# Kernel tuning notes

Hardware: AMD Instinct MI355X
Metric: run time of the kernel (lower is better)

The kernel has to match this reference:

```python
import jax, jax.numpy as jnp
import numpy as np

B, L, LQ = 64, 4096, 128
D = 32        # input_dim (value channels)
ET = 128      # embed_time
NH = 1        # num_heads
H = 128       # nhidden
NC = 6        # n_classes


def _time_emb(tt, lin_w, lin_b, per_w, per_b):
    # tt [..., T] -> [..., T, ET]; cat(Linear(1,1)(t), sin(Linear(1,ET-1)(t)))
    tt = tt[..., None]
    out1 = tt * lin_w[0, 0] + lin_b
    out2 = jnp.sin(tt @ per_w + per_b)
    return jnp.concatenate([out1, out2], axis=-1)


def _gru_dir(xs, wih, whh, bih, bhh, reverse):
    # xs [B, T, I] -> [B, T, H]; torch GRU gate math
    xs_t = jnp.swapaxes(xs, 0, 1)              # [T, B, I]
    if reverse:
        xs_t = xs_t[::-1]
    gi_all = xs_t @ wih.T + bih                # [T, B, 3H] precomputed input gates
    h0 = jnp.zeros((xs.shape[0], H), xs.dtype)

    def step(h, gi):
        gh = h @ whh.T + bhh
        ir, iz, inn = jnp.split(gi, 3, axis=-1)
        hr, hz, hn = jnp.split(gh, 3, axis=-1)
        r = jax.nn.sigmoid(ir + hr)
        z = jax.nn.sigmoid(iz + hz)
        n = jnp.tanh(inn + r * hn)
        h_new = (1.0 - z) * n + z * h
        return h_new, h_new

    _, ys = jax.lax.scan(step, h0, gi_all)     # [T, B, H]
    if reverse:
        ys = ys[::-1]
    return jnp.swapaxes(ys, 0, 1)


def _bigru(xs, wih, whh, bih, bhh):
    fwd = _gru_dir(xs, wih[0], whh[0], bih[0], bhh[0], False)
    bwd = _gru_dir(xs, wih[1], whh[1], bih[1], bhh[1], True)
    return jnp.concatenate([fwd, bwd], axis=-1)


def setup_inputs() -> dict:
    ks = jax.random.split(jax.random.key(0), 32)
    w = lambda i, s: jax.random.normal(ks[i], s, jnp.float32) * 0.05
    G3 = 3 * H
    return {
        "x": jax.random.normal(ks[0], (B, L, D), jnp.float32),
        "time_steps": jax.random.uniform(ks[1], (B, L), dtype=jnp.float32),
        "query_times": jnp.linspace(0.0, 1.0, LQ, dtype=jnp.float32),
        "lin_w": w(2, (1, 1)), "lin_b": w(3, (1,)),
        "per_w": w(4, (1, ET - 1)), "per_b": w(5, (ET - 1,)),
        "wq": w(6, (ET, ET)), "bq": w(7, (ET,)),
        "wk": w(8, (ET, ET)), "bk": w(9, (ET,)),
        "wo": w(10, (NH * D, H)), "bo": w(11, (H,)),
        "gru0_wih": w(12, (2, G3, H)), "gru0_whh": w(13, (2, G3, H)),
        "gru0_bih": w(14, (2, G3)), "gru0_bhh": w(15, (2, G3)),
        "gru1_wih": w(16, (2, G3, 2 * H)), "gru1_whh": w(17, (2, G3, H)),
        "gru1_bih": w(18, (2, G3)), "gru1_bhh": w(19, (2, G3)),
        "c1_w": w(20, (2 * H, 128)), "c1_b": w(21, (128,)),
        "c2_w": w(22, (128, 64)), "c2_b": w(23, (64,)),
        "c3_w": w(24, (64, NC)), "c3_b": w(25, (NC,)),
    }


def reference(x, time_steps, query_times, lin_w, lin_b, per_w, per_b,
              wq, bq, wk, bk, wo, bo,
              gru0_wih, gru0_whh, gru0_bih, gru0_bhh,
              gru1_wih, gru1_whh, gru1_bih, gru1_bhh,
              c1_w, c1_b, c2_w, c2_b, c3_w, c3_b):
    ek = ET // NH
    # learned time embeddings
    q = _time_emb(query_times[None, :], lin_w, lin_b, per_w, per_b)  # [1, LQ, ET]
    k = _time_emb(time_steps, lin_w, lin_b, per_w, per_b)            # [B, L, ET]
    # per-head projections
    qp = (q @ wq + bq).reshape(1, LQ, NH, ek).transpose(0, 2, 1, 3)[0]  # [NH, LQ, ek]
    kp = (k @ wk + bk).reshape(B, L, NH, ek).transpose(0, 2, 1, 3)      # [B, NH, L, ek]
    # mTAN attention: scores are channel-independent (mask=None), so the
    # per-channel repeat+softmax reduces to a single softmax over keys.
    scores = jnp.einsum('hqe,bhke->bhqk', qp, kp) / jnp.sqrt(jnp.float32(ek))
    p = jax.nn.softmax(scores, axis=-1)                                 # [B, NH, LQ, L]
    att = jnp.einsum('bhqk,bkd->bqhd', p, x).reshape(B, LQ, NH * D)
    att_out = att @ wo + bo                                             # [B, LQ, H]
    # 2-layer bidirectional GRU
    g0 = _bigru(att_out, gru0_wih, gru0_whh, gru0_bih, gru0_bhh)        # [B, LQ, 2H]
    g1 = _bigru(g0, gru1_wih, gru1_whh, gru1_bih, gru1_bhh)             # [B, LQ, 2H]
    class_in = jnp.concatenate([g1[:, -1, :H], g1[:, 0, H:]], axis=1)   # [B, 2H]
    out = ((class_in @ c1_w + c1_b) @ c2_w + c2_b) @ c3_w + c3_b        # [B, NC]
    return out
```

## Files before the change

### kernel.cpp

```cpp
#include <hip/hip_runtime.h>
#include <math.h>

#define Bn   64
#define Ln   4096
#define LQn  128
#define Dn   32
#define ETn  128
#define Hn   128
#define G3n  384
#define NDEG 12

typedef __attribute__((ext_vector_type(2))) float f32x2;
typedef __attribute__((ext_vector_type(2))) _Float16 f16x2;

#define DPPF(x, ctrl) __int_as_float(__builtin_amdgcn_update_dpp(0, __float_as_int(x), (ctrl), 0xF, 0xF, true))
#define QP_XOR1 0xB1
#define QP_XOR2 0x4E
#define QP_B0   0x00
#define QP_B1   0x55
#define QP_B2   0xAA
#define QP_B3   0xFF

__device__ __forceinline__ float sin_poly(float x) {
    const float x2 = x * x;
    float r = -1.9841270114e-04f;
    r = fmaf(r, x2,  8.3333337680e-03f);
    r = fmaf(r, x2, -1.6666667163e-01f);
    return fmaf(r * x2, x, x);
}
__device__ __forceinline__ float cos_poly(float x) {
    const float x2 = x * x;
    float r =  2.4801587642e-05f;
    r = fmaf(r, x2, -1.3888888899e-03f);
    r = fmaf(r, x2,  4.1666667908e-02f);
    r = fmaf(r, x2, -5.0000000000e-01f);
    return fmaf(r, x2, 1.0f);
}

#define WS_C    0
#define WS_WT   4096
#define WS_B2   (WS_WT + 768*32)
#define WS_CLS  (WS_B2 + 1024)
#define WS_G0   (WS_CLS + Bn*2*Hn)
#define WS_GI   (WS_G0 + Bn*LQn*2*Hn)
#define WS_ACCP WS_G0
#define WS_SP   (WS_G0 + 1048576)

__global__ __launch_bounds__(128) void k_coef(
    const float* __restrict__ qtimes, const float* __restrict__ lin_w,
    const float* __restrict__ lin_b, const float* __restrict__ per_w,
    const float* __restrict__ per_b, const float* __restrict__ wq,
    const float* __restrict__ bq, const float* __restrict__ wk,
    const float* __restrict__ bk, float* __restrict__ C)
{
    __shared__ float qe[ETn], qp_l[ETn], qt_l[ETn], bas[NDEG * 128], red[96], qbk_red[32];
    const int q = blockIdx.x, tid = threadIdx.x;
    if (tid < ETn - 1) {
        const float w = per_w[tid], bb = per_b[tid];
        const float sb = sin_poly(bb), cb = cos_poly(bb);
        float wp = 1.f;
#pragma unroll
        for (int d = 0; d < NDEG; ++d) {
            const float sd = ((d & 3) == 0) ? sb : ((d & 3) == 1) ? cb : ((d & 3) == 2) ? -sb : -cb;
            bas[d * 128 + tid] = wp * sd;
            wp *= w / (float)(d + 1);
        }
    }
    const float t = qtimes[q];
    qe[tid] = (tid == 0) ? fmaf(t, lin_w[0], lin_b[0])
                         : sin_poly(fmaf(t, per_w[tid - 1], per_b[tid - 1]));
    __syncthreads();
    {
        float a = bq[tid];
#pragma unroll 16
        for (int i = 0; i < ETn; ++i) a = fmaf(qe[i], wq[i * ETn + tid], a);
        qp_l[tid] = a;
    }
    __syncthreads();
    {
        const float4* wk4 = (const float4*)(wk + (size_t)tid * ETn);
        const float4* qp4 = (const float4*)qp_l;
        float a = 0.f;
#pragma unroll
        for (int k = 0; k < 32; ++k) {
            const float4 w4 = wk4[k], p4 = qp4[k];
            a += w4.x * p4.x + w4.y * p4.y + w4.z * p4.z + w4.w * p4.w;
        }
        qt_l[tid] = a;
    }
    __syncthreads();
    if (tid < 96) {
        const int d = tid >> 3, g = tid & 7;
        float p = 0.f;
        for (int j = g; j < ETn - 1; j += 8) p = fmaf(qt_l[j + 1], bas[d * 128 + j], p);
        red[tid] = p;
    } else {
        const int g2 = tid - 96;
        float p = 0.f;
#pragma unroll
        for (int k = 0; k < 4; ++k) p = fmaf(qp_l[g2 + 32 * k], bk[g2 + 32 * k], p);
        qbk_red[g2] = p;
    }
    __syncthreads();
    if (tid < NDEG) {
        const int d = tid;
        float s = red[d * 8 + 0] + red[d * 8 + 1] + red[d * 8 + 2] + red[d * 8 + 3]
                + red[d * 8 + 4] + red[d * 8 + 5] + red[d * 8 + 6] + red[d * 8 + 7];
        if (d == 0) {
            float qbk = 0.f;
#pragma unroll
            for (int k = 0; k < 32; ++k) qbk += qbk_red[k];
            s += qt_l[0] * lin_b[0] + qbk;
        }
        if (d == 1) s += qt_l[0] * lin_w[0];
        C[q * NDEG + d] = s * 0.08838834764831845f;
    }
}

__global__ __launch_bounds__(256) void k_fuse(
    const float* __restrict__ wih, const float* __restrict__ wo,
    const float* __restrict__ bo, const float* __restrict__ bih,
    float* __restrict__ Wt, float* __restrict__ bias2)
{
    const int t = blockIdx.x * 256 + threadIdx.x;
    if (t < 768 * 32) {
        const int o = t >> 5, d = t & 31;
        const float4* wr4 = (const float4*)(wih + (size_t)o * 128);
        const float4* wc4 = (const float4*)(wo + (size_t)d * 128);
        float a = 0.f;
#pragma unroll
        for (int k = 0; k < 32; ++k) {
            const float4 r4 = wr4[k], c4 = wc4[k];
            a += r4.x * c4.x + r4.y * c4.y + r4.z * c4.z + r4.w * c4.w;
        }
        Wt[t] = a;
    } else if (t < 768 * 33) {
        const int o = t - 768 * 32;
        const float4* wr4 = (const float4*)(wih + (size_t)o * 128);
        const float4* bo4 = (const float4*)bo;
        float a = bih[o];
#pragma unroll
        for (int k = 0; k < 32; ++k) {
            const float4 r4 = wr4[k], b4 = bo4[k];
            a += r4.x * b4.x + r4.y * b4.y + r4.z * b4.z + r4.w * b4.w;
        }
        bias2[o] = a;
    }
}

__global__ __launch_bounds__(512, 4) void k_attn(
    const float* __restrict__ x, const float* __restrict__ tsteps,
    const float* __restrict__ Cc, float* __restrict__ accP, float* __restrict__ sP)
{
    __shared__ __align__(16) char smem[4 * 128 * 36 * 4];
    float4* xls  = (float4*)smem;
    float*  slabf = (float*)smem;
#define SLAB(s, qq, c) slabf[(((s) * 128) + (qq)) * 36 + (c)]
    const int tid = threadIdx.x;
    const int b = blockIdx.x >> 2, lsplit = blockIdx.x & 3;
    const int i = tid & 3, qt = (tid >> 2) & 31, ls2 = tid >> 7;
    const int qown = 4 * qt + i;
    const int u = tid & 127;

    float c[NDEG];
#pragma unroll
    for (int d = 0; d < NDEG; ++d) c[d] = Cc[qown * NDEG + d];

    const int l0 = lsplit * 1024 + ls2 * 256;
    const float4* tg4 = (const float4*)(tsteps + (size_t)b * Ln + l0);
    const float4* xg  = (const float4*)(x + ((size_t)b * Ln + l0) * Dn);

    f32x2 acc2[4][4];
#pragma unroll
    for (int m = 0; m < 4; ++m)
#pragma unroll
        for (int e = 0; e < 4; ++e) { acc2[m][e].x = 0.f; acc2[m][e].y = 0.f; }
    float s_own = 0.f;

    float4 xr[4];
#pragma unroll
    for (int w = 0; w < 4; ++w) xr[w] = xg[u + 128 * w];

    for (int ch = 0; ch < 4; ++ch) {
        __syncthreads();
#pragma unroll
        for (int w = 0; w < 4; ++w) xls[ls2 * 512 + u + 128 * w] = xr[w];
        __syncthreads();
        if (ch < 3) {
            const int off = (ch + 1) * 512;
#pragma unroll
            for (int w = 0; w < 4; ++w) xr[w] = xg[off + u + 128 * w];
        }
        const float4* xrow = &xls[ls2 * 512];
        for (int k = 0; k < 16; ++k) {
            const float4 t4 = tg4[ch * 16 + k];
#pragma unroll
            for (int jj = 0; jj < 4; ++jj) {
                const float t = (jj == 0) ? t4.x : (jj == 1) ? t4.y : (jj == 2) ? t4.z : t4.w;
                float sc = c[NDEG - 1];
#pragma unroll
                for (int d = NDEG - 2; d >= 0; --d) sc = fmaf(sc, t, c[d]);
                const float pe = __expf(sc);
                s_own += pe;
                const float p0 = DPPF(pe, QP_B0);
                const float p1 = DPPF(pe, QP_B1);
                const float p2 = DPPF(pe, QP_B2);
                const float p3 = DPPF(pe, QP_B3);
                const int lrow = (k * 4 + jj) * 8;
                const float4 xa = xrow[lrow + 2 * i];
                const float4 xb = xrow[lrow + 2 * i + 1];
                f32x2 xa0; xa0.x = xa.x; xa0.y = xa.y;
                f32x2 xa1; xa1.x = xa.z; xa1.y = xa.w;
                f32x2 xb0; xb0.x = xb.x; xb0.y = xb.y;
                f32x2 xb1; xb1.x = xb.z; xb1.y = xb.w;
#define PKA(m, pv) { f32x2 pp; pp.x = (pv); pp.y = (pv); \
    acc2[m][0] = __builtin_elementwise_fma(pp, xa0, acc2[m][0]); \
    acc2[m][1] = __builtin_elementwise_fma(pp, xa1, acc2[m][1]); \
    acc2[m][2] = __builtin_elementwise_fma(pp, xb0, acc2[m][2]); \
    acc2[m][3] = __builtin_elementwise_fma(pp, xb1, acc2[m][3]); }
                PKA(0, p0) PKA(1, p1) PKA(2, p2) PKA(3, p3)
#undef PKA
            }
        }
    }
    __syncthreads();
#pragma unroll
    for (int m = 0; m < 4; ++m) {
        float4 f4a, f4b;
        f4a.x = acc2[m][0].x; f4a.y = acc2[m][0].y; f4a.z = acc2[m][1].x; f4a.w = acc2[m][1].y;
        f4b.x = acc2[m][2].x; f4b.y = acc2[m][2].y; f4b.z = acc2[m][3].x; f4b.w = acc2[m][3].y;
        *(float4*)&SLAB(ls2, 4 * qt + m, 8 * i)     = f4a;
        *(float4*)&SLAB(ls2, 4 * qt + m, 8 * i + 4) = f4b;
    }
    SLAB(ls2, qown, 32) = s_own;
    __syncthreads();
    const int q = tid & 127, part = tid >> 7;
#pragma unroll
    for (int j = 0; j < 2; ++j) {
        const int off = (part * 2 + j) * 4;
        float4 r  = *(float4*)&SLAB(0, q, off);
        float4 r1 = *(float4*)&SLAB(1, q, off);
        float4 r2 = *(float4*)&SLAB(2, q, off);
        float4 r3 = *(float4*)&SLAB(3, q, off);
        r.x += r1.x + r2.x + r3.x; r.y += r1.y + r2.y + r3.y;
        r.z += r1.z + r2.z + r3.z; r.w += r1.w + r2.w + r3.w;
        *(float4*)&accP[((((size_t)lsplit * Bn + b) * LQn + q) * 32) + off] = r;
    }
    if (part == 0) {
        sP[((size_t)lsplit * Bn + b) * LQn + q] =
            SLAB(0, q, 32) + SLAB(1, q, 32) + SLAB(2, q, 32) + SLAB(3, q, 32);
    }
#undef SLAB
}

__global__ __launch_bounds__(256) void k_gemm_att(
    const float* __restrict__ accP, const float* __restrict__ sP,
    const float* __restrict__ Bm, const float* __restrict__ bias,
    float* __restrict__ Cm)
{
    __shared__ float4 A_l[64 * 8];
    __shared__ float4 B_l[64 * 8];
    const int tid = threadIdx.x;
    const int m0 = blockIdx.x * 64, n0 = blockIdx.y * 64;
    const int r0 = (tid >> 4) << 2, c0 = (tid & 15) << 2;
    f32x2 acc2[4][4];
#pragma unroll
    for (int a = 0; a < 4; ++a)
#pragma unroll
        for (int bb = 0; bb < 4; ++bb) { acc2[a][bb].x = 0.f; acc2[a][bb].y = 0.f; }
    const float4* Ag = (const float4*)accP;
    const float4* Bg = (const float4*)Bm;

#pragma unroll
    for (int w = 0; w < 2; ++w) {
        const int idx = tid + w * 256;
        const int row = idx >> 3, c4 = idx & 7;
        const int sc = (c4 + row + (row >> 2)) & 7;
        const int m = m0 + row;
        float4 a0 = Ag[(size_t)m * 8 + c4];
        float4 a1 = Ag[((size_t)8192  + m) * 8 + c4];
        float4 a2 = Ag[((size_t)16384 + m) * 8 + c4];
        float4 a3 = Ag[((size_t)24576 + m) * 8 + c4];
        const float inv = 1.f / (sP[m] + sP[8192 + m] + sP[16384 + m] + sP[24576 + m]);
        float4 av;
        av.x = (a0.x + a1.x + a2.x + a3.x) * inv;
        av.y = (a0.y + a1.y + a2.y + a3.y) * inv;
        av.z = (a0.z + a1.z + a2.z + a3.z) * inv;
        av.w = (a0.w + a1.w + a2.w + a3.w) * inv;
        A_l[row * 8 + sc] = av;
        B_l[row * 8 + sc] = Bg[(size_t)(n0 + row) * 8 + c4];
    }
    __syncthreads();
#pragma unroll
    for (int k4 = 0; k4 < 8; ++k4) {
        float4 av[4], bv[4];
#pragma unroll
        for (int j = 0; j < 4; ++j) {
            const int ra = r0 + j;
            av[j] = A_l[ra * 8 + ((k4 + ra + (ra >> 2)) & 7)];
        }
#pragma unroll
        for (int j = 0; j < 4; ++j) {
            const int rb = c0 + j;
            bv[j] = B_l[rb * 8 + ((k4 + rb + (rb >> 2)) & 7)];
        }
#pragma unroll
        for (int ri = 0; ri < 4; ++ri) {
            f32x2 alo; alo.x = av[ri].x; alo.y = av[ri].y;
            f32x2 ahi; ahi.x = av[ri].z; ahi.y = av[ri].w;
#pragma unroll
            for (int ci = 0; ci < 4; ++ci) {
                f32x2 blo; blo.x = bv[ci].x; blo.y = bv[ci].y;
                f32x2 bhi; bhi.x = bv[ci].z; bhi.y = bv[ci].w;
                acc2[ri][ci] = __builtin_elementwise_fma(alo, blo, acc2[ri][ci]);
                acc2[ri][ci] = __builtin_elementwise_fma(ahi, bhi, acc2[ri][ci]);
            }
        }
    }
#pragma unroll
    for (int ri = 0; ri < 4; ++ri) {
        float4 o4;
        o4.x = acc2[ri][0].x + acc2[ri][0].y + bias[n0 + c0 + 0];
        o4.y = acc2[ri][1].x + acc2[ri][1].y + bias[n0 + c0 + 1];
        o4.z = acc2[ri][2].x + acc2[ri][2].y + bias[n0 + c0 + 2];
        o4.w = acc2[ri][3].x + acc2[ri][3].y + bias[n0 + c0 + 3];
        *(float4*)&Cm[(size_t)(m0 + r0 + ri) * 768 + n0 + c0] = o4;
    }
}

__global__ __launch_bounds__(256) void k_gemm_nt(
    const float* __restrict__ A, const float* __restrict__ Bm,
    const float* __restrict__ bias, float* __restrict__ Cm,
    int N, int K)
{
    __shared__ float4 A_l[64 * 8];
    __shared__ float4 B_l[64 * 8];
    const int tid = threadIdx.x;
    const int m0 = blockIdx.x * 64, n0 = blockIdx.y * 64;
    const int r0 = (tid >> 4) << 2, c0 = (tid & 15) << 2;
    const int K4 = K >> 2;
    f32x2 acc2[4][4];
#pragma unroll
    for (int a = 0; a < 4; ++a)
#pragma unroll
        for (int bb = 0; bb < 4; ++bb) { acc2[a][bb].x = 0.f; acc2[a][bb].y = 0.f; }
    const float4* Ag = (const float4*)A;
    const float4* Bg = (const float4*)Bm;

    for (int k0 = 0; k0 < K4; k0 += 8) {
        __syncthreads();
#pragma unroll
        for (int w = 0; w < 2; ++w) {
            const int idx = tid + w * 256;
            const int row = idx >> 3, c4 = idx & 7;
            const int sc = (c4 + row + (row >> 2)) & 7;
            A_l[row * 8 + sc] = Ag[(size_t)(m0 + row) * K4 + k0 + c4];
            B_l[row * 8 + sc] = Bg[(size_t)(n0 + row) * K4 + k0 + c4];
        }
        __syncthreads();
#pragma unroll
        for (int k4 = 0; k4 < 8; ++k4) {
            float4 av[4], bv[4];
#pragma unroll
            for (int j = 0; j < 4; ++j) {
                const int ra = r0 + j;
                av[j] = A_l[ra * 8 + ((k4 + ra + (ra >> 2)) & 7)];
            }
#pragma unroll
            for (int j = 0; j < 4; ++j) {
                const int rb = c0 + j;
                bv[j] = B_l[rb * 8 + ((k4 + rb + (rb >> 2)) & 7)];
            }
#pragma unroll
            for (int ri = 0; ri < 4; ++ri) {
                f32x2 alo; alo.x = av[ri].x; alo.y = av[ri].y;
                f32x2 ahi; ahi.x = av[ri].z; ahi.y = av[ri].w;
#pragma unroll
                for (int ci = 0; ci < 4; ++ci) {
                    f32x2 blo; blo.x = bv[ci].x; blo.y = bv[ci].y;
                    f32x2 bhi; bhi.x = bv[ci].z; bhi.y = bv[ci].w;
                    acc2[ri][ci] = __builtin_elementwise_fma(alo, blo, acc2[ri][ci]);
                    acc2[ri][ci] = __builtin_elementwise_fma(ahi, bhi, acc2[ri][ci]);
                }
            }
        }
    }
#pragma unroll
    for (int ri = 0; ri < 4; ++ri) {
        float4 o4;
        o4.x = acc2[ri][0].x + acc2[ri][0].y + bias[n0 + c0 + 0];
        o4.y = acc2[ri][1].x + acc2[ri][1].y + bias[n0 + c0 + 1];
        o4.z = acc2[ri][2].x + acc2[ri][2].y + bias[n0 + c0 + 2];
        o4.w = acc2[ri][3].x + acc2[ri][3].y + bias[n0 + c0 + 3];
        *(float4*)&Cm[(size_t)(m0 + r0 + ri) * N + n0 + c0] = o4;
    }
}

__global__ __launch_bounds__(256, 1) void k_gru(
    const float* __restrict__ gi, const float* __restrict__ whh,
    const float* __restrict__ bhh, float* __restrict__ seq_out,
    float* __restrict__ final_out)
{
    __shared__ _Float16 h16[2][Hn];
    __shared__ float    h32[2][Hn];
    const int tid = threadIdx.x;
    const int b = blockIdx.x >> 1, dir = blockIdx.x & 1;
    const int j = tid >> 1, q = tid & 1;

    f16x2 wr[32], wz[32], wn[32];
    {
        const float* wb = whh + ((size_t)dir * G3n + j) * Hn + 64 * q;
        const f32x2* p0 = (const f32x2*)(wb);
        const f32x2* p1 = (const f32x2*)(wb + (size_t)128 * Hn);
        const f32x2* p2 = (const f32x2*)(wb + (size_t)256 * Hn);
#pragma unroll
        for (int k = 0; k < 32; ++k) {
            f32x2 a = p0[k], z2 = p1[k], c2 = p2[k];
            wr[k].x = (_Float16)a.x;  wr[k].y = (_Float16)a.y;
            wz[k].x = (_Float16)z2.x; wz[k].y = (_Float16)z2.y;
            wn[k].x = (_Float16)c2.x; wn[k].y = (_Float16)c2.y;
        }
    }
#pragma unroll
    for (int k = 0; k < 32; ++k) {
        asm volatile("" : "+v"(wr[k]));
        asm volatile("" : "+v"(wz[k]));
        asm volatile("" : "+v"(wn[k]));
    }
    const float bhr = bhh[dir * G3n + j];
    const float bhz = bhh[dir * G3n + 128 + j];
    const float bhn = bhh[dir * G3n + 256 + j];

    if (tid < Hn) {
        h32[0][tid] = 0.f; h32[1][tid] = 0.f;
        h16[0][tid] = (_Float16)0.f; h16[1][tid] = (_Float16)0.f;
    }
    __syncthreads();

    const long sstride = dir ? -768 : 768;
    const float* gptr = gi + (size_t)b * LQn * 768 + dir * G3n + j
                        + (size_t)(dir ? LQn - 1 : 0) * 768;

    int cur = 0;
    float hlast = 0.f;

    auto gstep = [&](const float gir, const float giz, const float gin, const int step) {
        const float hold = h32[cur][j];
        const float4* hb4 = (const float4*)(&h16[cur][64 * q]);
        float srA = 0.f, szA = 0.f, snA = 0.f;
        float srB = 0.f, szB = 0.f, snB = 0.f;
#pragma unroll
        for (int k2 = 0; k2 < 4; ++k2) {
            float4 hv = hb4[k2];
            f16x2 h0 = *(f16x2*)&hv.x;
            f16x2 h1 = *(f16x2*)&hv.y;
            f16x2 h2 = *(f16x2*)&hv.z;
            f16x2 h3 = *(f16x2*)&hv.w;
            asm("v_dot2_f32_f16 %0, %1, %2, %0" : "+v"(srA) : "v"(wr[4 * k2 + 0]), "v"(h0));
            asm("v_dot2_f32_f16 %0, %1, %2, %0" : "+v"(szA) : "v"(wz[4 * k2 + 0]), "v"(h0));
            asm("v_dot2_f32_f16 %0, %1, %2, %0" : "+v"(snA) : "v"(wn[4 * k2 + 0]), "v"(h0));
            asm("v_dot2_f32_f16 %0, %1, %2, %0" : "+v"(srA) : "v"(wr[4 * k2 + 1]), "v"(h1));
            asm("v_dot2_f32_f16 %0, %1, %2, %0" : "+v"(szA) : "v"(wz[4 * k2 + 1]), "v"(h1));
            asm("v_dot2_f32_f16 %0, %1, %2, %0" : "+v"(snA) : "v"(wn[4 * k2 + 1]), "v"(h1));
            asm("v_dot2_f32_f16 %0, %1, %2, %0" : "+v"(srA) : "v"(wr[4 * k2 + 2]), "v"(h2));
            asm("v_dot2_f32_f16 %0, %1, %2, %0" : "+v"(szA) : "v"(wz[4 * k2 + 2]), "v"(h2));
            asm("v_dot2_f32_f16 %0, %1, %2, %0" : "+v"(snA) : "v"(wn[4 * k2 + 2]), "v"(h2));
            asm("v_dot2_f32_f16 %0, %1, %2, %0" : "+v"(srA) : "v"(wr[4 * k2 + 3]), "v"(h3));
            asm("v_dot2_f32_f16 %0, %1, %2, %0" : "+v"(szA) : "v"(wz[4 * k2 + 3]), "v"(h3));
            asm("v_dot2_f32_f16 %0, %1, %2, %0" : "+v"(snA) : "v"(wn[4 * k2 + 3]), "v"(h3));
        }
#pragma unroll
        for (int k2 = 4; k2 < 8; ++k2) {
            float4 hv = hb4[k2];
            f16x2 h0 = *(f16x2*)&hv.x;
            f16x2 h1 = *(f16x2*)&hv.y;
            f16x2 h2 = *(f16x2*)&hv.z;
            f16x2 h3 = *(f16x2*)&hv.w;
            asm("v_dot2_f32_f16 %0, %1, %2, %0" : "+v"(srB) : "v"(wr[4 * k2 + 0]), "v"(h0));
            asm("v_dot2_f32_f16 %0, %1, %2, %0" : "+v"(szB) : "v"(wz[4 * k2 + 0]), "v"(h0));
            asm("v_dot2_f32_f16 %0, %1, %2, %0" : "+v"(snB) : "v"(wn[4 * k2 + 0]), "v"(h0));
            asm("v_dot2_f32_f16 %0, %1, %2, %0" : "+v"(srB) : "v"(wr[4 * k2 + 1]), "v"(h1));
            asm("v_dot2_f32_f16 %0, %1, %2, %0" : "+v"(szB) : "v"(wz[4 * k2 + 1]), "v"(h1));
            asm("v_dot2_f32_f16 %0, %1, %2, %0" : "+v"(snB) : "v"(wn[4 * k2 + 1]), "v"(h1));
            asm("v_dot2_f32_f16 %0, %1, %2, %0" : "+v"(srB) : "v"(wr[4 * k2 + 2]), "v"(h2));
            asm("v_dot2_f32_f16 %0, %1, %2, %0" : "+v"(szB) : "v"(wz[4 * k2 + 2]), "v"(h2));
            asm("v_dot2_f32_f16 %0, %1, %2, %0" : "+v"(snB) : "v"(wn[4 * k2 + 2]), "v"(h2));
            asm("v_dot2_f32_f16 %0, %1, %2, %0" : "+v"(srB) : "v"(wr[4 * k2 + 3]), "v"(h3));
            asm("v_dot2_f32_f16 %0, %1, %2, %0" : "+v"(szB) : "v"(wz[4 * k2 + 3]), "v"(h3));
            asm("v_dot2_f32_f16 %0, %1, %2, %0" : "+v"(snB) : "v"(wn[4 * k2 + 3]), "v"(h3));
        }
        float sr = srA + srB, sz = szA + szB, sn = snA + snB;
        sr += DPPF(sr, QP_XOR1);
        sz += DPPF(sz, QP_XOR1);
        sn += DPPF(sn, QP_XOR1);
        const float r = 1.f / (1.f + __expf(-(gir + sr + bhr)));
        const float z = 1.f / (1.f + __expf(-(giz + sz + bhz)));
        const float nx = gin + r * (sn + bhn);
        const float n = 1.f - 2.f / (1.f + __expf(2.f * nx));
        const float hn = n + z * (hold - n);
        if (q == 0) {
            h32[cur ^ 1][j] = hn;
            h16[cur ^ 1][j] = (_Float16)hn;
            if (seq_out) {
                const int l = dir ? (LQn - 1 - step) : step;
                seq_out[((size_t)(b * LQn + l)) * (2 * Hn) + dir * Hn + j] = hn;
            }
        }
        hlast = hn;
        cur ^= 1;
        asm volatile("s_waitcnt lgkmcnt(0)\n\ts_barrier" ::: "memory");
    };

    float gA[3], gB[3];
#define GLD(dst, s) { const long o = (long)(s) * sstride; \
    dst[0] = gptr[o]; dst[1] = gptr[o + 128]; dst[2] = gptr[o + 256]; }
    GLD(gA, 0) GLD(gB, 1)
    for (int s0 = 0; s0 < LQn; s0 += 2) {
        gstep(gA[0], gA[1], gA[2], s0);
        { const int sn2 = (s0 + 2 < LQn) ? s0 + 2 : LQn - 1; GLD(gA, sn2) }
        gstep(gB[0], gB[1], gB[2], s0 + 1);
        { const int sn2 = (s0 + 3 < LQn) ? s0 + 3 : LQn - 1; GLD(gB, sn2) }
    }
#undef GLD
    if (final_out && q == 0) final_out[b * 2 * Hn + dir * Hn + j] = hlast;
}

__global__ __launch_bounds__(256) void k_cls(
    const float* __restrict__ cls_in,
    const float* __restrict__ c1w, const float* __restrict__ c1b,
    const float* __restrict__ c2w, const float* __restrict__ c2b,
    const float* __restrict__ c3w, const float* __restrict__ c3b,
    float* __restrict__ out)
{
    __shared__ float ci[256], y1[128], y2[64];
    const int b = blockIdx.x, tid = threadIdx.x;
    ci[tid] = cls_in[b * 256 + tid];
    __syncthreads();
    if (tid < 128) { float a = c1b[tid]; for (int i = 0; i < 256; ++i) a += ci[i] * c1w[i * 128 + tid]; y1[tid] = a; }
    __syncthreads();
    if (tid < 64)  { float a = c2b[tid]; for (int i = 0; i < 128; ++i) a += y1[i] * c2w[i * 64 + tid];  y2[tid] = a; }
    __syncthreads();
    if (tid < 6)   { float a = c3b[tid]; for (int i = 0; i < 64; ++i)  a += y2[i] * c3w[i * 6 + tid];   out[b * 6 + tid] = a; }
}

extern "C" void kernel_launch(void* const* d_in, const int* in_sizes, int n_in,
                              void* d_out, int out_size, void* d_ws, size_t ws_size,
                              hipStream_t stream)
{
    const float* x        = (const float*)d_in[0];
    const float* tsteps   = (const float*)d_in[1];
    const float* qtimes   = (const float*)d_in[2];
    const float* lin_w    = (const float*)d_in[3];
    const float* lin_b    = (const float*)d_in[4];
    const float* per_w    = (const float*)d_in[5];
    const float* per_b    = (const float*)d_in[6];
    const float* wq       = (const float*)d_in[7];
    const float* bq       = (const float*)d_in[8];
    const float* wk       = (const float*)d_in[9];
    const float* bk       = (const float*)d_in[10];
    const float* wo       = (const float*)d_in[11];
    const float* bo       = (const float*)d_in[12];
    const float* g0_wih   = (const float*)d_in[13];
    const float* g0_whh   = (const float*)d_in[14];
    const float* g0_bih   = (const float*)d_in[15];
    const float* g0_bhh   = (const float*)d_in[16];
    const float* g1_wih   = (const float*)d_in[17];
    const float* g1_whh   = (const float*)d_in[18];
    const float* g1_bih   = (const float*)d_in[19];
    const float* g1_bhh   = (const float*)d_in[20];
    const float* c1w      = (const float*)d_in[21];
    const float* c1b      = (const float*)d_in[22];
    const float* c2w      = (const float*)d_in[23];
    const float* c2b      = (const float*)d_in[24];
    const float* c3w      = (const float*)d_in[25];
    const float* c3b      = (const float*)d_in[26];
    float* out = (float*)d_out;
    float* ws  = (float*)d_ws;

    float* Cws   = ws + WS_C;
    float* Wt    = ws + WS_WT;
    float* bias2 = ws + WS_B2;
    float* clsin = ws + WS_CLS;
    float* g0buf = ws + WS_G0;
    float* accP  = ws + WS_ACCP;
    float* sPb   = ws + WS_SP;
    float* gibuf = ws + WS_GI;

    k_coef<<<128, 128, 0, stream>>>(qtimes, lin_w, lin_b, per_w, per_b, wq, bq, wk, bk, Cws);
    k_fuse<<<99, 256, 0, stream>>>(g0_wih, wo, bo, g0_bih, Wt, bias2);
    k_attn<<<256, 512, 0, stream>>>(x, tsteps, Cws, accP, sPb);

    k_gemm_att<<<dim3(128, 12), 256, 0, stream>>>(accP, sPb, Wt, bias2, gibuf);
    k_gru<<<128, 256, 0, stream>>>(gibuf, g0_whh, g0_bhh, g0buf, nullptr);

    k_gemm_nt<<<dim3(128, 12), 256, 0, stream>>>(g0buf, g1_wih, g1_bih, gibuf, 768, 256);
    k_gru<<<128, 256, 0, stream>>>(gibuf, g1_whh, g1_bhh, nullptr, clsin);

    k_cls<<<64, 256, 0, stream>>>(clsin, c1w, c1b, c2w, c2b, c3w, c3b, out);
}
```

Measured before the change: 288.7 us.

## Run layer-1 GRU input GEMM on fp16 MFMA with fp16 layer-0 outputs

Replaces the fp32 SIMT tiled GEMM for the second GRU layer's input projection with an MFMA 16x16x32 fp16 kernel that reads operands straight from global memory. The first GRU layer now writes its sequence output as fp16, and a new kernel converts the layer-1 input weights to fp16 on each call. This moves the GEMM onto matrix cores and halves the bytes read for activations and weights, at the cost of fp16 precision, an extra launch, and no LDS staging.

```diff
diff --git a/kernel.cpp b/kernel.cpp
--- a/kernel.cpp
+++ b/kernel.cpp
@@ -12,6 +12,8 @@
 
 typedef __attribute__((ext_vector_type(2))) float f32x2;
 typedef __attribute__((ext_vector_type(2))) _Float16 f16x2;
+typedef __attribute__((ext_vector_type(8))) _Float16 f16x8;
+typedef __attribute__((ext_vector_type(4))) float f32x4;
 
 #define DPPF(x, ctrl) __int_as_float(__builtin_amdgcn_update_dpp(0, __float_as_int(x), (ctrl), 0xF, 0xF, true))
 #define QP_XOR1 0xB1
@@ -45,6 +47,7 @@
 #define WS_GI   (WS_G0 + Bn*LQn*2*Hn)
 #define WS_ACCP WS_G0
 #define WS_SP   (WS_G0 + 1048576)
+#define WS_W16  (WS_G0 + 1100000)
 
 __global__ __launch_bounds__(128) void k_coef(
     const float* __restrict__ qtimes, const float* __restrict__ lin_w,
@@ -146,6 +149,13 @@
         }
         bias2[o] = a;
     }
+}
+
+__global__ __launch_bounds__(256) void k_w16(
+    const float* __restrict__ w, _Float16* __restrict__ w16)
+{
+    const int idx = blockIdx.x * 256 + threadIdx.x;
+    if (idx < 768 * 256) w16[idx] = (_Float16)w[idx];
 }
 
 __global__ __launch_bounds__(512, 4) void k_attn(
@@ -328,77 +338,49 @@
     }
 }
 
-__global__ __launch_bounds__(256) void k_gemm_nt(
-    const float* __restrict__ A, const float* __restrict__ Bm,
-    const float* __restrict__ bias, float* __restrict__ Cm,
-    int N, int K)
-{
-    __shared__ float4 A_l[64 * 8];
-    __shared__ float4 B_l[64 * 8];
+__global__ __launch_bounds__(256) void k_gemm16(
+    const _Float16* __restrict__ g0, const _Float16* __restrict__ w16,
+    const float* __restrict__ bias, float* __restrict__ Cm)
+{
     const int tid = threadIdx.x;
-    const int m0 = blockIdx.x * 64, n0 = blockIdx.y * 64;
-    const int r0 = (tid >> 4) << 2, c0 = (tid & 15) << 2;
-    const int K4 = K >> 2;
-    f32x2 acc2[4][4];
-#pragma unroll
-    for (int a = 0; a < 4; ++a)
-#pragma unroll
-        for (int bb = 0; bb < 4; ++bb) { acc2[a][bb].x = 0.f; acc2[a][bb].y = 0.f; }
-    const float4* Ag = (const float4*)A;
-    const float4* Bg = (const float4*)Bm;
-
-    for (int k0 = 0; k0 < K4; k0 += 8) {
-        __syncthreads();
-#pragma unroll
-        for (int w = 0; w < 2; ++w) {
-            const int idx = tid + w * 256;
-            const int row = idx >> 3, c4 = idx & 7;
-            const int sc = (c4 + row + (row >> 2)) & 7;
-            A_l[row * 8 + sc] = Ag[(size_t)(m0 + row) * K4 + k0 + c4];
-            B_l[row * 8 + sc] = Bg[(size_t)(n0 + row) * K4 + k0 + c4];
-        }
-        __syncthreads();
-#pragma unroll
-        for (int k4 = 0; k4 < 8; ++k4) {
-            float4 av[4], bv[4];
-#pragma unroll
-            for (int j = 0; j < 4; ++j) {
-                const int ra = r0 + j;
-                av[j] = A_l[ra * 8 + ((k4 + ra + (ra >> 2)) & 7)];
-            }
-#pragma unroll
-            for (int j = 0; j < 4; ++j) {
-                const int rb = c0 + j;
-                bv[j] = B_l[rb * 8 + ((k4 + rb + (rb >> 2)) & 7)];
-            }
-#pragma unroll
-            for (int ri = 0; ri < 4; ++ri) {
-                f32x2 alo; alo.x = av[ri].x; alo.y = av[ri].y;
-                f32x2 ahi; ahi.x = av[ri].z; ahi.y = av[ri].w;
-#pragma unroll
-                for (int ci = 0; ci < 4; ++ci) {
-                    f32x2 blo; blo.x = bv[ci].x; blo.y = bv[ci].y;
-                    f32x2 bhi; bhi.x = bv[ci].z; bhi.y = bv[ci].w;
-                    acc2[ri][ci] = __builtin_elementwise_fma(alo, blo, acc2[ri][ci]);
-                    acc2[ri][ci] = __builtin_elementwise_fma(ahi, bhi, acc2[ri][ci]);
-                }
-            }
-        }
-    }
-#pragma unroll
-    for (int ri = 0; ri < 4; ++ri) {
-        float4 o4;
-        o4.x = acc2[ri][0].x + acc2[ri][0].y + bias[n0 + c0 + 0];
-        o4.y = acc2[ri][1].x + acc2[ri][1].y + bias[n0 + c0 + 1];
-        o4.z = acc2[ri][2].x + acc2[ri][2].y + bias[n0 + c0 + 2];
-        o4.w = acc2[ri][3].x + acc2[ri][3].y + bias[n0 + c0 + 3];
-        *(float4*)&Cm[(size_t)(m0 + r0 + ri) * N + n0 + c0] = o4;
+    const int wave = tid >> 6, lane = tid & 63;
+    const int m0 = blockIdx.x * 64 + wave * 16;
+    const int n0 = blockIdx.y * 64;
+    const int koff = 8 * (lane >> 4);
+
+    const _Float16* Ab = g0 + (size_t)(m0 + (lane & 15)) * 256 + koff;
+    const _Float16* Bb0 = w16 + (size_t)(n0 +  0 + (lane & 15)) * 256 + koff;
+    const _Float16* Bb1 = w16 + (size_t)(n0 + 16 + (lane & 15)) * 256 + koff;
+    const _Float16* Bb2 = w16 + (size_t)(n0 + 32 + (lane & 15)) * 256 + koff;
+    const _Float16* Bb3 = w16 + (size_t)(n0 + 48 + (lane & 15)) * 256 + koff;
+
+    f32x4 acc0 = {0.f, 0.f, 0.f, 0.f}, acc1 = acc0, acc2 = acc0, acc3 = acc0;
+#pragma unroll
+    for (int k0 = 0; k0 < 256; k0 += 32) {
+        const f16x8 a  = *(const f16x8*)(Ab  + k0);
+        const f16x8 b0 = *(const f16x8*)(Bb0 + k0);
+        const f16x8 b1 = *(const f16x8*)(Bb1 + k0);
+        const f16x8 b2 = *(const f16x8*)(Bb2 + k0);
+        const f16x8 b3 = *(const f16x8*)(Bb3 + k0);
+        acc0 = __builtin_amdgcn_mfma_f32_16x16x32_f16(a, b0, acc0, 0, 0, 0);
+        acc1 = __builtin_amdgcn_mfma_f32_16x16x32_f16(a, b1, acc1, 0, 0, 0);
+        acc2 = __builtin_amdgcn_mfma_f32_16x16x32_f16(a, b2, acc2, 0, 0, 0);
+        acc3 = __builtin_amdgcn_mfma_f32_16x16x32_f16(a, b3, acc3, 0, 0, 0);
+    }
+    const int mr = m0 + (lane >> 4) * 4;
+    const int nc = lane & 15;
+#pragma unroll
+    for (int r = 0; r < 4; ++r) {
+        Cm[(size_t)(mr + r) * 768 + n0 +  0 + nc] = acc0[r] + bias[n0 +  0 + nc];
+        Cm[(size_t)(mr + r) * 768 + n0 + 16 + nc] = acc1[r] + bias[n0 + 16 + nc];
+        Cm[(size_t)(mr + r) * 768 + n0 + 32 + nc] = acc2[r] + bias[n0 + 32 + nc];
+        Cm[(size_t)(mr + r) * 768 + n0 + 48 + nc] = acc3[r] + bias[n0 + 48 + nc];
     }
 }
 
 __global__ __launch_bounds__(256, 1) void k_gru(
     const float* __restrict__ gi, const float* __restrict__ whh,
-    const float* __restrict__ bhh, float* __restrict__ seq_out,
+    const float* __restrict__ bhh, _Float16* __restrict__ seq_out,
     float* __restrict__ final_out)
 {
     __shared__ _Float16 h16[2][Hn];
@@ -503,7 +485,7 @@
             h16[cur ^ 1][j] = (_Float16)hn;
             if (seq_out) {
                 const int l = dir ? (LQn - 1 - step) : step;
-                seq_out[((size_t)(b * LQn + l)) * (2 * Hn) + dir * Hn + j] = hn;
+                seq_out[((size_t)(b * LQn + l)) * (2 * Hn) + dir * Hn + j] = (_Float16)hn;
             }
         }
         hlast = hn;
@@ -581,19 +563,21 @@
     float* Wt    = ws + WS_WT;
     float* bias2 = ws + WS_B2;
     float* clsin = ws + WS_CLS;
-    float* g0buf = ws + WS_G0;
     float* accP  = ws + WS_ACCP;
     float* sPb   = ws + WS_SP;
     float* gibuf = ws + WS_GI;
+    _Float16* g0f16 = (_Float16*)(ws + WS_G0);
+    _Float16* w16b  = (_Float16*)(ws + WS_W16);
 
     k_coef<<<128, 128, 0, stream>>>(qtimes, lin_w, lin_b, per_w, per_b, wq, bq, wk, bk, Cws);
     k_fuse<<<99, 256, 0, stream>>>(g0_wih, wo, bo, g0_bih, Wt, bias2);
     k_attn<<<256, 512, 0, stream>>>(x, tsteps, Cws, accP, sPb);
 
     k_gemm_att<<<dim3(128, 12), 256, 0, stream>>>(accP, sPb, Wt, bias2, gibuf);
-    k_gru<<<128, 256, 0, stream>>>(gibuf, g0_whh, g0_bhh, g0buf, nullptr);
-
-    k_gemm_nt<<<dim3(128, 12), 256, 0, stream>>>(g0buf, g1_wih, g1_bih, gibuf, 768, 256);
+    k_w16<<<768, 256, 0, stream>>>(g1_wih, w16b);
+    k_gru<<<128, 256, 0, stream>>>(gibuf, g0_whh, g0_bhh, g0f16, nullptr);
+
+    k_gemm16<<<dim3(128, 12), 256, 0, stream>>>(g0f16, w16b, g1_bih, gibuf);
     k_gru<<<128, 256, 0, stream>>>(gibuf, g1_whh, g1_bhh, nullptr, clsin);
 
     k_cls<<<64, 256, 0, stream>>>(clsin, c1w, c1b, c2w, c2b, c3w, c3b, out);
```

Result: faster. 274.5 us (-4.9%).
